# Optimization experiments

Hardware: AMD Instinct MI355X
Metric: run time of the kernel (lower is better)

## Reference

```python
import jax, jax.numpy as jnp
import numpy as np

D = 768
H = 16
DH = D // H  # 48
SCALE = 1.0 / np.sqrt(DH).astype(np.float32)
EPS = 1e-3  # keras LayerNormalization default epsilon
NEG = -1e9


def setup_inputs() -> dict:
    key = jax.random.key(0)
    ks = jax.random.split(key, 10)
    B, S = 4, 2048
    q = jax.random.normal(ks[0], (B, S, D), dtype=jnp.float32)
    k = jax.random.normal(ks[1], (B, S, D), dtype=jnp.float32)
    v = jax.random.normal(ks[2], (B, S, D), dtype=jnp.float32)
    # Dense projection params (glorot-ish scale)
    w_std = 1.0 / np.sqrt(D)
    Wq = jax.random.normal(ks[3], (D, D), dtype=jnp.float32) * w_std
    Wk = jax.random.normal(ks[4], (D, D), dtype=jnp.float32) * w_std
    Wv = jax.random.normal(ks[5], (D, D), dtype=jnp.float32) * w_std
    bq = jnp.zeros((D,), jnp.float32)
    bk = jnp.zeros((D,), jnp.float32)
    bv = jnp.zeros((D,), jnp.float32)
    gamma = jnp.ones((D,), jnp.float32)
    beta = jnp.zeros((D,), jnp.float32)
    return {"q": q, "k": k, "v": v, "Wq": Wq, "bq": bq, "Wk": Wk, "bk": bk,
            "Wv": Wv, "bv": bv, "gamma": gamma, "beta": beta}


def reference(q, k, v, Wq, bq, Wk, bk, Wv, bv, gamma, beta):
    use_causal = True  # exercise the causal-mask path
    B, S, _ = q.shape
    # Projections, then split into heads (tf.split on last axis == reshape)
    Q = (q @ Wq + bq).reshape(B, S, H, DH)
    K = (k @ Wk + bk).reshape(B, S, H, DH)
    V = (v @ Wv + bv).reshape(B, S, H, DH)
    # scores: [B, H, Sq, Sk]
    scores = jnp.einsum('bqhd,bkhd->bhqk', Q, K) * SCALE
    if use_causal:
        qi = jnp.arange(S)[:, None]
        ki = jnp.arange(S)[None, :]
        mask = jnp.where(qi >= ki, 0.0, NEG).astype(scores.dtype)
        scores = scores + mask
    attn = jax.nn.softmax(scores, axis=-1)
    out = jnp.einsum('bhqk,bkhd->bqhd', attn, V).reshape(B, S, D)
    # LayerNorm over last dim
    mu = jnp.mean(out, axis=-1, keepdims=True)
    var = jnp.mean(jnp.square(out - mu), axis=-1, keepdims=True)
    return (out - mu) * jax.lax.rsqrt(var + EPS) * gamma + beta
```

## Files before the change

### kernel.cpp

```cpp
#include <hip/hip_runtime.h>
#include <hip/hip_bf16.h>


#define DMODEL 768
#define NHEAD  16
#define DHEAD  48
#define SEQ    2048
#define NBATCH 4
#define NROWS  (NBATCH * SEQ)
#define QSCALE (0.14433756729740643f * 1.4426950408889634f)

typedef __bf16 bf16x8 __attribute__((ext_vector_type(8)));
typedef float  f32x4  __attribute__((ext_vector_type(4)));

#define GLDS16(g, l) __builtin_amdgcn_global_load_lds(                         \
    (const __attribute__((address_space(1))) unsigned int*)(g),                \
    (__attribute__((address_space(3))) unsigned int*)(l), 16, 0, 0)

__global__ __launch_bounds__(256) void transpose_w(
    const float* __restrict__ Wq,
    const float* __restrict__ Wk,
    const float* __restrict__ Wv,
    __hip_bfloat16* __restrict__ Wt)
{
    __shared__ __hip_bfloat16 tile[32][33];
    int bid = blockIdx.x;
    int mat = bid / 576;
    int t   = bid - mat * 576;
    int tr  = t / 24, tc = t - (t / 24) * 24;
    const float* W = (mat == 0) ? Wq : (mat == 1) ? Wk : Wv;
    __hip_bfloat16* O = Wt + (size_t)mat * DMODEL * DMODEL;
    int tx = threadIdx.x & 31, ty = threadIdx.x >> 5;
#pragma unroll
    for (int i = 0; i < 32; i += 8)
        tile[ty + i][tx] = __float2bfloat16(W[(size_t)(tr * 32 + ty + i) * DMODEL + tc * 32 + tx]);
    __syncthreads();
#pragma unroll
    for (int i = 0; i < 32; i += 8)
        O[(size_t)(tc * 32 + ty + i) * DMODEL + tr * 32 + tx] = tile[tx][ty + i];
}

__global__ __launch_bounds__(256) void qkv_proj(
    const float* __restrict__ xq,
    const float* __restrict__ xk,
    const float* __restrict__ xv,
    const __hip_bfloat16* __restrict__ Wt,
    const float* __restrict__ bq,
    const float* __restrict__ bk,
    const float* __restrict__ bv,
    __hip_bfloat16* __restrict__ Qr,
    __hip_bfloat16* __restrict__ Kr,
    __hip_bfloat16* __restrict__ Vt)
{
    __shared__ __hip_bfloat16 As[128 * 32];
    __shared__ __hip_bfloat16 Bs[128 * 32];

    int xcd  = blockIdx.x & 7;
    int s    = blockIdx.x >> 3;
    int nt   = s % 6;
    int pair = (s / 6) * 8 + xcd;
    int mat  = pair >> 6;
    int mt   = pair & 63;
    int m0   = mt * 128, n0 = nt * 128;

    const float* X          = (mat == 0) ? xq : (mat == 1) ? xk : xv;
    const __hip_bfloat16* W = Wt + (size_t)mat * DMODEL * DMODEL;
    const float* bias       = (mat == 0) ? bq : (mat == 1) ? bk : bv;

    int tid  = threadIdx.x;
    int w    = tid >> 6, lane = tid & 63;
    int l16  = lane & 15, quad = lane >> 4;
    int wm   = w >> 1, wn = w & 1;

    int rowA = tid >> 2;
    int offA = (tid & 3) * 8;

    const float* xb0 = X + (size_t)(m0 + rowA) * DMODEL + offA;
    const float* xb1 = X + (size_t)(m0 + 64 + rowA) * DMODEL + offA;
    const __hip_bfloat16* wb0 = W + (size_t)(n0 + rowA) * DMODEL + offA;
    const __hip_bfloat16* wb1 = W + (size_t)(n0 + 64 + rowA) * DMODEL + offA;

    f32x4 acc[4][4] = {};

    for (int k0 = 0; k0 < DMODEL; k0 += 32) {
        __syncthreads();
        GLDS16(wb0 + k0, &Bs[tid * 8]);
        GLDS16(wb1 + k0, &Bs[2048 + tid * 8]);
        {
            float4 f0 = *(const float4*)(xb0 + k0);
            float4 f1 = *(const float4*)(xb0 + k0 + 4);
            float4 g0 = *(const float4*)(xb1 + k0);
            float4 g1 = *(const float4*)(xb1 + k0 + 4);
            *(bf16x8*)&As[tid * 8] =
                (bf16x8){ (__bf16)f0.x, (__bf16)f0.y, (__bf16)f0.z, (__bf16)f0.w,
                          (__bf16)f1.x, (__bf16)f1.y, (__bf16)f1.z, (__bf16)f1.w };
            *(bf16x8*)&As[2048 + tid * 8] =
                (bf16x8){ (__bf16)g0.x, (__bf16)g0.y, (__bf16)g0.z, (__bf16)g0.w,
                          (__bf16)g1.x, (__bf16)g1.y, (__bf16)g1.z, (__bf16)g1.w };
        }
        __syncthreads();

        bf16x8 a[4], b[4];
#pragma unroll
        for (int i = 0; i < 4; ++i)
            a[i] = *(const bf16x8*)&As[(wm * 64 + i * 16 + l16) * 32 + quad * 8];
#pragma unroll
        for (int j = 0; j < 4; ++j)
            b[j] = *(const bf16x8*)&Bs[(wn * 64 + j * 16 + l16) * 32 + quad * 8];
#pragma unroll
        for (int i = 0; i < 4; ++i)
#pragma unroll
            for (int j = 0; j < 4; ++j)
                acc[i][j] = __builtin_amdgcn_mfma_f32_16x16x32_bf16(a[i], b[j], acc[i][j], 0, 0, 0);
    }

#pragma unroll
    for (int j = 0; j < 4; ++j) {
        int col = n0 + wn * 64 + j * 16 + l16;
        float bc = bias[col];
        if (mat == 0) {
#pragma unroll
            for (int i = 0; i < 4; ++i) {
                int row0 = m0 + wm * 64 + i * 16 + quad * 4;
#pragma unroll
                for (int r = 0; r < 4; ++r)
                    Qr[(size_t)(row0 + r) * DMODEL + col] =
                        __float2bfloat16((acc[i][j][r] + bc) * QSCALE);
            }
        } else if (mat == 1) {
#pragma unroll
            for (int i = 0; i < 4; ++i) {
                int row0 = m0 + wm * 64 + i * 16 + quad * 4;
#pragma unroll
                for (int r = 0; r < 4; ++r)
                    Kr[(size_t)(row0 + r) * DMODEL + col] =
                        __float2bfloat16(acc[i][j][r] + bc);
            }
        } else {
            int h = col / 48, dh = col - h * 48;
#pragma unroll
            for (int i = 0; i < 4; ++i) {
                int row0 = m0 + wm * 64 + i * 16 + quad * 4;
                int bb = row0 >> 11, s0 = row0 & 2047;
                ushort4 pk;
                union { __hip_bfloat16 b; unsigned short u; } cv;
                cv.b = __float2bfloat16(acc[i][j][0] + bc); pk.x = cv.u;
                cv.b = __float2bfloat16(acc[i][j][1] + bc); pk.y = cv.u;
                cv.b = __float2bfloat16(acc[i][j][2] + bc); pk.z = cv.u;
                cv.b = __float2bfloat16(acc[i][j][3] + bc); pk.w = cv.u;
                *(ushort4*)(Vt + ((size_t)(bb * NHEAD + h) * DHEAD + dh) * SEQ + s0) = pk;
            }
        }
    }
}

__global__ __launch_bounds__(256) void attn(
    const __hip_bfloat16* __restrict__ Qr,
    const __hip_bfloat16* __restrict__ Kr,
    const __hip_bfloat16* __restrict__ Vt,
    __hip_bfloat16* __restrict__ Ao)
{
    __shared__ __hip_bfloat16 Ks[2][64][72];
    __shared__ __hip_bfloat16 Vs[2][48][72];
    __shared__ __hip_bfloat16 Ps[4][32][72];

    int tid  = threadIdx.x;
    int w    = tid >> 6, lane = tid & 63;
    int l16  = lane & 15, quad = lane >> 4;
    int bh   = blockIdx.x & 63;
    int qt   = 15 - (blockIdx.x >> 6);
    int q0   = qt * 128;
    int b    = bh >> 4, h = bh & 15;
    size_t rowbase = (size_t)b * SEQ;

    const __hip_bfloat16* Qp = Qr + rowbase * DMODEL + h * DHEAD;
    const __hip_bfloat16* Kp = Kr + rowbase * DMODEL + h * DHEAD;
    const __hip_bfloat16* Vp = Vt + (size_t)bh * DHEAD * SEQ;

    for (int idx = tid; idx < 1024; idx += 256) {
        int buf = idx >> 9, r = (idx >> 3) & 63, c = idx & 7;
        ((unsigned int*)&Ks[buf][r][48])[c] = 0u;
    }

    bf16x8 bQ0[2], bQ1[2];
#pragma unroll
    for (int i = 0; i < 2; ++i) {
        int qrow = q0 + w * 32 + i * 16 + l16;
        bQ0[i] = *(const bf16x8*)(Qp + (size_t)qrow * DMODEL + quad * 8);
        bQ1[i] = (bf16x8){};
        if (quad < 2)
            bQ1[i] = *(const bf16x8*)(Qp + (size_t)qrow * DMODEL + 32 + quad * 8);
    }

    int rK = tid >> 2, oK = (tid & 3) * 12;
    int dV = tid >> 3, oV = (tid & 7) * 8;

    uint2 kr0, kr1, kr2; uint4 vr0, vr1;

#define ATTN_LOAD(kt_) {                                                        \
        int k0_ = (kt_) * 64;                                                   \
        const __hip_bfloat16* kb_ = Kp + (size_t)(k0_ + rK) * DMODEL + oK;      \
        kr0 = *(const uint2*)(kb_);                                             \
        kr1 = *(const uint2*)(kb_ + 4);                                         \
        kr2 = *(const uint2*)(kb_ + 8);                                         \
        vr0 = *(const uint4*)(Vp + (size_t)dV * SEQ + k0_ + oV);                \
        if (tid < 128) vr1 = *(const uint4*)(Vp + (size_t)(32 + dV) * SEQ + k0_ + oV); }

#define ATTN_STORE(buf_) {                                                      \
        __hip_bfloat16* kd_ = &Ks[buf_][rK][oK];                                \
        *(uint2*)(kd_)     = kr0;                                               \
        *(uint2*)(kd_ + 4) = kr1;                                               \
        *(uint2*)(kd_ + 8) = kr2;                                               \
        *(uint4*)&Vs[buf_][dV][oV] = vr0;                                       \
        if (tid < 128) *(uint4*)&Vs[buf_][32 + dV][oV] = vr1; }

    f32x4 O[2][3] = {};
    float lsum[2] = {0.f, 0.f};

    int ktmax = 2 * qt + 1;
    ATTN_LOAD(0);
    ATTN_STORE(0);
    if (ktmax >= 1) ATTN_LOAD(1);
    __syncthreads();

    for (int kt = 0; kt <= ktmax; ++kt) {
        int buf = kt & 1;
        int k0  = kt * 64;
        if (kt + 1 <= ktmax) ATTN_STORE(buf ^ 1);
        if (kt + 2 <= ktmax) ATTN_LOAD(kt + 2);

        bf16x8 aK0[4], aK1[4];
#pragma unroll
        for (int t = 0; t < 4; ++t) {
            aK0[t] = *(const bf16x8*)&Ks[buf][16 * t + l16][quad * 8];
            aK1[t] = *(const bf16x8*)&Ks[buf][16 * t + l16][32 + quad * 8];
        }

#pragma unroll
        for (int i = 0; i < 2; ++i) {
            int qbase = q0 + w * 32 + i * 16;
            if (k0 > qbase + 15) continue;

            f32x4 s[4];
#pragma unroll
            for (int t = 0; t < 4; ++t) {
                f32x4 z = {};
                z    = __builtin_amdgcn_mfma_f32_16x16x32_bf16(aK0[t], bQ0[i], z, 0, 0, 0);
                s[t] = __builtin_amdgcn_mfma_f32_16x16x32_bf16(aK1[t], bQ1[i], z, 0, 0, 0);
            }

            if (k0 + 63 > qbase) {
                int qg = qbase + l16;
#pragma unroll
                for (int t = 0; t < 4; ++t) {
                    int kg = k0 + 16 * t + quad * 4;
#pragma unroll
                    for (int r = 0; r < 4; ++r)
                        if (kg + r > qg) s[t][r] = -1e30f;
                }
            }

            float ls = 0.f;
#pragma unroll
            for (int t = 0; t < 4; ++t) {
                float p0 = exp2f(s[t][0]), p1 = exp2f(s[t][1]);
                float p2 = exp2f(s[t][2]), p3 = exp2f(s[t][3]);
                ls += (p0 + p1) + (p2 + p3);
                union { __bf16 hv[4]; uint2 u2; } pk;
                pk.hv[0] = (__bf16)p0; pk.hv[1] = (__bf16)p1;
                pk.hv[2] = (__bf16)p2; pk.hv[3] = (__bf16)p3;
                *(uint2*)&Ps[w][i * 16 + l16][16 * t + quad * 4] = pk.u2;
            }
            lsum[i] += ls;
        }

        bf16x8 bV0[3], bV1[3];
#pragma unroll
        for (int dt = 0; dt < 3; ++dt) {
            bV0[dt] = *(const bf16x8*)&Vs[buf][dt * 16 + l16][quad * 8];
            bV1[dt] = *(const bf16x8*)&Vs[buf][dt * 16 + l16][32 + quad * 8];
        }

#pragma unroll
        for (int i = 0; i < 2; ++i) {
            int qbase = q0 + w * 32 + i * 16;
            if (k0 > qbase + 15) continue;
            bf16x8 aP0 = *(const bf16x8*)&Ps[w][i * 16 + l16][quad * 8];
            bf16x8 aP1 = *(const bf16x8*)&Ps[w][i * 16 + l16][32 + quad * 8];
#pragma unroll
            for (int dt = 0; dt < 3; ++dt) {
                O[i][dt] = __builtin_amdgcn_mfma_f32_16x16x32_bf16(aP0, bV0[dt], O[i][dt], 0, 0, 0);
                O[i][dt] = __builtin_amdgcn_mfma_f32_16x16x32_bf16(aP1, bV1[dt], O[i][dt], 0, 0, 0);
            }
        }

        __syncthreads();
    }

#pragma unroll
    for (int i = 0; i < 2; ++i) {
        lsum[i] += __shfl_xor(lsum[i], 16, 64);
        lsum[i] += __shfl_xor(lsum[i], 32, 64);
    }

#pragma unroll
    for (int i = 0; i < 2; ++i) {
#pragma unroll
        for (int r = 0; r < 4; ++r) {
            float linv = 1.f / __shfl(lsum[i], quad * 4 + r, 64);
            size_t g = (rowbase + q0 + w * 32 + i * 16 + quad * 4 + r) * DMODEL + h * DHEAD + l16;
            Ao[g + 0]  = __float2bfloat16(O[i][0][r] * linv);
            Ao[g + 16] = __float2bfloat16(O[i][1][r] * linv);
            Ao[g + 32] = __float2bfloat16(O[i][2][r] * linv);
        }
    }
#undef ATTN_LOAD
#undef ATTN_STORE
}

__global__ __launch_bounds__(192) void lnorm(
    const __hip_bfloat16* __restrict__ Ao,
    const float* __restrict__ gamma,
    const float* __restrict__ beta,
    float* __restrict__ out)
{
    __shared__ float rs_[3], rq_[3];
    int row = blockIdx.x;
    int t   = threadIdx.x;
    size_t base = (size_t)row * DMODEL + t * 4;

    ushort4 u = *(const ushort4*)(Ao + base);
    float x0, x1, x2, x3;
    { unsigned int v = (unsigned int)u.x << 16; __builtin_memcpy(&x0, &v, 4); }
    { unsigned int v = (unsigned int)u.y << 16; __builtin_memcpy(&x1, &v, 4); }
    { unsigned int v = (unsigned int)u.z << 16; __builtin_memcpy(&x2, &v, 4); }
    { unsigned int v = (unsigned int)u.w << 16; __builtin_memcpy(&x3, &v, 4); }

    float s = x0 + x1 + x2 + x3;
    float q = x0 * x0 + x1 * x1 + x2 * x2 + x3 * x3;
#pragma unroll
    for (int m = 32; m >= 1; m >>= 1) {
        s += __shfl_xor(s, m, 64);
        q += __shfl_xor(q, m, 64);
    }
    int wv = t >> 6;
    if ((t & 63) == 0) { rs_[wv] = s; rq_[wv] = q; }
    __syncthreads();
    float ts = rs_[0] + rs_[1] + rs_[2];
    float tq = rq_[0] + rq_[1] + rq_[2];
    float mu  = ts * (1.f / 768.f);
    float var = tq * (1.f / 768.f) - mu * mu;
    float rstd = rsqrtf(var + 1e-3f);

    float4 g  = *(const float4*)(gamma + t * 4);
    float4 be = *(const float4*)(beta + t * 4);
    float4 o;
    o.x = (x0 - mu) * rstd * g.x + be.x;
    o.y = (x1 - mu) * rstd * g.y + be.y;
    o.z = (x2 - mu) * rstd * g.z + be.z;
    o.w = (x3 - mu) * rstd * g.w + be.w;
    *(float4*)(out + base) = o;
}

extern "C" void kernel_launch(void* const* d_in, const int* in_sizes, int n_in,
                              void* d_out, int out_size, void* d_ws, size_t ws_size,
                              hipStream_t stream) {
    const float* q     = (const float*)d_in[0];
    const float* k     = (const float*)d_in[1];
    const float* v     = (const float*)d_in[2];
    const float* Wq    = (const float*)d_in[3];
    const float* bq    = (const float*)d_in[4];
    const float* Wk    = (const float*)d_in[5];
    const float* bk    = (const float*)d_in[6];
    const float* Wv    = (const float*)d_in[7];
    const float* bv    = (const float*)d_in[8];
    const float* gamma = (const float*)d_in[9];
    const float* beta  = (const float*)d_in[10];

    char* basep = (char*)d_ws;
    __hip_bfloat16* Wt = (__hip_bfloat16*)basep;
    __hip_bfloat16* Qr = (__hip_bfloat16*)(basep + 3538944);
    __hip_bfloat16* Kr = Qr + (size_t)NROWS * DMODEL;
    __hip_bfloat16* Vt = Kr + (size_t)NROWS * DMODEL;
    __hip_bfloat16* Ao = Vt + (size_t)NROWS * DMODEL;
    float* out = (float*)d_out;

    hipLaunchKernelGGL(transpose_w, dim3(1728), dim3(256), 0, stream, Wq, Wk, Wv, Wt);
    hipLaunchKernelGGL(qkv_proj, dim3(1152), dim3(256), 0, stream,
                       q, k, v, Wt, bq, bk, bv, Qr, Kr, Vt);
    hipLaunchKernelGGL(attn, dim3(1024), dim3(256), 0, stream, Qr, Kr, Vt, Ao);
    hipLaunchKernelGGL(lnorm, dim3(8192), dim3(192), 0, stream, Ao, gamma, beta, out);
}
```

Baseline: 272.3 us.

## Double-buffer LDS tiles with register prefetch in QKV projection GEMM

Replaces the single-buffered LDS tiles and direct global-to-LDS loads in the QKV projection with double-buffered LDS and a register-staged prefetch two k-steps ahead. The next tile is written to the alternate buffer while MFMAs run on the current one, so each iteration needs one barrier instead of two and global load latency is hidden behind compute. In exchange it doubles LDS use, holds the prefetched tile in registers, and drops the global_load_lds path for weights. It also changes the thread-to-row mapping so each thread loads 16 contiguous elements of one row.

```diff
diff --git a/kernel.cpp b/kernel.cpp
--- a/kernel.cpp
+++ b/kernel.cpp
@@ -12,10 +12,6 @@
 
 typedef __bf16 bf16x8 __attribute__((ext_vector_type(8)));
 typedef float  f32x4  __attribute__((ext_vector_type(4)));
-
-#define GLDS16(g, l) __builtin_amdgcn_global_load_lds(                         \
-    (const __attribute__((address_space(1))) unsigned int*)(g),                \
-    (__attribute__((address_space(3))) unsigned int*)(l), 16, 0, 0)
 
 __global__ __launch_bounds__(256) void transpose_w(
     const float* __restrict__ Wq,
@@ -52,8 +48,8 @@
     __hip_bfloat16* __restrict__ Kr,
     __hip_bfloat16* __restrict__ Vt)
 {
-    __shared__ __hip_bfloat16 As[128 * 32];
-    __shared__ __hip_bfloat16 Bs[128 * 32];
+    __shared__ __hip_bfloat16 As[2][128 * 32];
+    __shared__ __hip_bfloat16 Bs[2][128 * 32];
 
     int xcd  = blockIdx.x & 7;
     int s    = blockIdx.x >> 3;
@@ -72,47 +68,62 @@
     int l16  = lane & 15, quad = lane >> 4;
     int wm   = w >> 1, wn = w & 1;
 
-    int rowA = tid >> 2;
-    int offA = (tid & 3) * 8;
-
-    const float* xb0 = X + (size_t)(m0 + rowA) * DMODEL + offA;
-    const float* xb1 = X + (size_t)(m0 + 64 + rowA) * DMODEL + offA;
-    const __hip_bfloat16* wb0 = W + (size_t)(n0 + rowA) * DMODEL + offA;
-    const __hip_bfloat16* wb1 = W + (size_t)(n0 + 64 + rowA) * DMODEL + offA;
+    int rS = tid >> 1;
+    int cS = (tid & 1) << 4;
+    const float*          xb = X + (size_t)(m0 + rS) * DMODEL + cS;
+    const __hip_bfloat16* wb = W + (size_t)(n0 + rS) * DMODEL + cS;
+    int ldsOff = rS * 32 + cS;
+
+    float4 fA0, fA1, fA2, fA3;
+    uint4  rB0, rB1;
+
+#define QKV_LOAD(k0_) {                                                        \
+        fA0 = *(const float4*)(xb + (k0_));                                    \
+        fA1 = *(const float4*)(xb + (k0_) + 4);                                \
+        fA2 = *(const float4*)(xb + (k0_) + 8);                                \
+        fA3 = *(const float4*)(xb + (k0_) + 12);                               \
+        rB0 = *(const uint4*)(wb + (k0_));                                     \
+        rB1 = *(const uint4*)(wb + (k0_) + 8); }
+
+#define QKV_STORE(buf_) {                                                      \
+        *(bf16x8*)&As[buf_][ldsOff] =                                          \
+            (bf16x8){ (__bf16)fA0.x, (__bf16)fA0.y, (__bf16)fA0.z, (__bf16)fA0.w, \
+                      (__bf16)fA1.x, (__bf16)fA1.y, (__bf16)fA1.z, (__bf16)fA1.w }; \
+        *(bf16x8*)&As[buf_][ldsOff + 8] =                                      \
+            (bf16x8){ (__bf16)fA2.x, (__bf16)fA2.y, (__bf16)fA2.z, (__bf16)fA2.w, \
+                      (__bf16)fA3.x, (__bf16)fA3.y, (__bf16)fA3.z, (__bf16)fA3.w }; \
+        *(uint4*)&Bs[buf_][ldsOff]     = rB0;                                  \
+        *(uint4*)&Bs[buf_][ldsOff + 8] = rB1; }
 
     f32x4 acc[4][4] = {};
 
-    for (int k0 = 0; k0 < DMODEL; k0 += 32) {
-        __syncthreads();
-        GLDS16(wb0 + k0, &Bs[tid * 8]);
-        GLDS16(wb1 + k0, &Bs[2048 + tid * 8]);
-        {
-            float4 f0 = *(const float4*)(xb0 + k0);
-            float4 f1 = *(const float4*)(xb0 + k0 + 4);
-            float4 g0 = *(const float4*)(xb1 + k0);
-            float4 g1 = *(const float4*)(xb1 + k0 + 4);
-            *(bf16x8*)&As[tid * 8] =
-                (bf16x8){ (__bf16)f0.x, (__bf16)f0.y, (__bf16)f0.z, (__bf16)f0.w,
-                          (__bf16)f1.x, (__bf16)f1.y, (__bf16)f1.z, (__bf16)f1.w };
-            *(bf16x8*)&As[2048 + tid * 8] =
-                (bf16x8){ (__bf16)g0.x, (__bf16)g0.y, (__bf16)g0.z, (__bf16)g0.w,
-                          (__bf16)g1.x, (__bf16)g1.y, (__bf16)g1.z, (__bf16)g1.w };
-        }
-        __syncthreads();
+    QKV_LOAD(0);
+    QKV_STORE(0);
+    QKV_LOAD(32);
+    __syncthreads();
+
+    for (int it = 0; it < 24; ++it) {
+        int buf = it & 1;
+        if (it + 1 < 24) QKV_STORE(buf ^ 1);
+        if (it + 2 < 24) QKV_LOAD((it + 2) * 32);
 
         bf16x8 a[4], b[4];
 #pragma unroll
         for (int i = 0; i < 4; ++i)
-            a[i] = *(const bf16x8*)&As[(wm * 64 + i * 16 + l16) * 32 + quad * 8];
+            a[i] = *(const bf16x8*)&As[buf][(wm * 64 + i * 16 + l16) * 32 + quad * 8];
 #pragma unroll
         for (int j = 0; j < 4; ++j)
-            b[j] = *(const bf16x8*)&Bs[(wn * 64 + j * 16 + l16) * 32 + quad * 8];
+            b[j] = *(const bf16x8*)&Bs[buf][(wn * 64 + j * 16 + l16) * 32 + quad * 8];
 #pragma unroll
         for (int i = 0; i < 4; ++i)
 #pragma unroll
             for (int j = 0; j < 4; ++j)
                 acc[i][j] = __builtin_amdgcn_mfma_f32_16x16x32_bf16(a[i], b[j], acc[i][j], 0, 0, 0);
-    }
+
+        __syncthreads();
+    }
+#undef QKV_LOAD
+#undef QKV_STORE
 
 #pragma unroll
     for (int j = 0; j < 4; ++j) {
```

Measured after the change: 275.1 us. No clear change (+1.0%).
